# Kernel tuning notes

Hardware: AMD Instinct MI355X
Metric: run time of the kernel (lower is better)

## Reference

```python
import jax, jax.numpy as jnp
import numpy as np

N_NODES = 50000
N_EDGES = 1000000


def _edge_conv(x, src, dst, W, b, n_nodes):
    """PyG EdgeConv: msg = nn(cat([x_i, x_j - x_i])), aggr=max over incoming edges."""
    xi = x[dst]                      # [E, C] target features
    xj = x[src]                      # [E, C] source features
    m = jnp.concatenate([xi, xj - xi], axis=-1)          # [E, 2C]
    m = jax.nn.relu(m @ W + b)                           # [E, C_out]
    out = jax.ops.segment_max(m, dst, num_segments=n_nodes)  # [N, C_out]
    # empty segments produce -inf; PyG fills with 0
    return jnp.where(jnp.isfinite(out), out, 0.0)


def setup_inputs() -> dict:
    key = jax.random.key(0)
    ks = jax.random.split(key, 12)
    x = jax.random.normal(ks[0], (N_NODES, 3), dtype=jnp.float32)
    edge_index = jax.random.randint(ks[1], (2, N_EDGES), 0, N_NODES, dtype=jnp.int64)

    def lin(k, fan_in, fan_out):
        s = 1.0 / np.sqrt(fan_in)
        kw, kb = jax.random.split(k)
        W = jax.random.uniform(kw, (fan_in, fan_out), jnp.float32, -s, s)
        b = jax.random.uniform(kb, (fan_out,), jnp.float32, -s, s)
        return W, b

    W1, b1 = lin(ks[2], 6, 64)       # conv1 MLP([3*2, 64])
    W2, b2 = lin(ks[3], 128, 128)    # conv2 MLP([64*2, 128])
    W3, b3 = lin(ks[4], 256, 512)    # conv3 MLP([128*2, 512])
    W4, b4 = lin(ks[5], 512, 256)    # lin1 MLP([512, 256])
    W5, b5 = lin(ks[6], 256, 3)      # lin1 final Linear(256, 3)
    return {"x": x, "edge_index": edge_index,
            "W1": W1, "b1": b1, "W2": W2, "b2": b2, "W3": W3, "b3": b3,
            "W4": W4, "b4": b4, "W5": W5, "b5": b5}


def reference(x, edge_index, W1, b1, W2, b2, W3, b3, W4, b4, W5, b5):
    src = edge_index[0]  # x_j
    dst = edge_index[1]  # x_i (aggregation target)
    n = x.shape[0]
    x1 = _edge_conv(x, src, dst, W1, b1, n)    # [N, 64]
    x2 = _edge_conv(x1, src, dst, W2, b2, n)   # [N, 128]
    x3 = _edge_conv(x2, src, dst, W3, b3, n)   # [N, 512]
    x4 = jax.nn.relu(x3 @ W4 + b4) @ W5 + b5   # [N, 3]
    return x + x4
```

## Files before the change

kernel.cpp:

```cpp
#include <hip/hip_runtime.h>

static constexpr int NN = 50000;
static constexpr int NE = 1000000;

typedef short bf16x8 __attribute__((ext_vector_type(8)));
typedef float f32x4 __attribute__((ext_vector_type(4)));
typedef unsigned short u16x2 __attribute__((ext_vector_type(2)));

__device__ inline float bf2f_raw(unsigned short u) {
    return __uint_as_float(((unsigned int)u) << 16);
}
__device__ inline unsigned short f2bf(float f) {
    unsigned int u = __float_as_uint(f);
    u += 0x7fffu + ((u >> 16) & 1u);
    return (unsigned short)(u >> 16);
}
__device__ inline unsigned short f2bfs(float f) {
    unsigned short b = f2bf(f);
    return (b & 0x8000u) ? (unsigned short)(~b) : (unsigned short)(b | 0x8000u);
}
__device__ inline float unsrt2f(unsigned short v) {
    unsigned short b = (v & 0x8000u) ? (unsigned short)(v ^ 0x8000u)
                                     : (unsigned short)(~v);
    return bf2f_raw(b);
}
__device__ inline unsigned int pkmax(unsigned int a, unsigned int b) {
    u16x2 r = __builtin_elementwise_max(__builtin_bit_cast(u16x2, a),
                                        __builtin_bit_cast(u16x2, b));
    return __builtin_bit_cast(unsigned int, r);
}
__device__ inline uint4 pkmax4(uint4 a, uint4 b) {
    a.x = pkmax(a.x, b.x); a.y = pkmax(a.y, b.y);
    a.z = pkmax(a.z, b.z); a.w = pkmax(a.w, b.w);
    return a;
}
__device__ inline unsigned int pack2(float f0, float f1) {
    return (unsigned int)f2bf(f0) | ((unsigned int)f2bf(f1) << 16);
}
__device__ inline unsigned int addrelu2t(unsigned int a, unsigned int t) {
    float t0 = unsrt2f((unsigned short)(t & 0xffffu));
    float t1 = unsrt2f((unsigned short)(t >> 16));
    float f0 = fmaxf(bf2f_raw((unsigned short)(a & 0xffffu)) + t0, 0.f);
    float f1 = fmaxf(bf2f_raw((unsigned short)(a >> 16)) + t1, 0.f);
    return pack2(f0, f1);
}


__global__ void setup_kernel(const float* __restrict__ x, const float* __restrict__ W1,
                             const float* __restrict__ b1, const float* __restrict__ b5,
                             const float* __restrict__ W2, const float* __restrict__ W3,
                             const float* __restrict__ W4,
                             unsigned short* __restrict__ as1, float* __restrict__ out,
                             int* __restrict__ deg, int* __restrict__ cursor,
                             unsigned short* __restrict__ Bt2,
                             unsigned short* __restrict__ Bt3,
                             unsigned short* __restrict__ W4t) {
    int t = blockIdx.x * blockDim.x + threadIdx.x;
    if (t < NN * 128) {
        int i = t >> 7, c = t & 127;
        float x0 = x[i * 3 + 0], x1 = x[i * 3 + 1], x2 = x[i * 3 + 2];
        if (c < 64) {
            float v = x0 * (W1[c] - W1[192 + c]) + x1 * (W1[64 + c] - W1[256 + c]) +
                      x2 * (W1[128 + c] - W1[320 + c]) + b1[c];
            as1[t] = f2bf(v);
        } else {
            int cs = c - 64;
            float v = x0 * W1[192 + cs] + x1 * W1[256 + cs] + x2 * W1[320 + cs];
            as1[t] = f2bfs(v);
        }
        return;
    }
    t -= NN * 128;
    if (t < NN * 3) { out[t] = x[t] + b5[t % 3]; return; }
    t -= NN * 3;
    if (t < NN) { deg[t] = 0; return; }
    t -= NN;
    if (t < NN) { cursor[t] = 0; return; }
    t -= NN;
    if (t < 8192) {
        int k = t / 128, c = t % 128;
        float wt = W2[k * 128 + c];
        float wb = W2[(64 + k) * 128 + c];
        Bt2[c * 64 + k] = f2bf(wt - wb);
        Bt2[(128 + c) * 64 + k] = f2bf(wb);
        return;
    }
    t -= 8192;
    if (t < 65536) {
        int k = t / 512, c = t % 512;
        float wt = W3[k * 512 + c];
        float wb = W3[(128 + k) * 512 + c];
        Bt3[c * 128 + k] = f2bf(wt - wb);
        Bt3[(512 + c) * 128 + k] = f2bf(wb);
        return;
    }
    t -= 65536;
    if (t < 131072) {
        int k = t / 256, n = t % 256;
        W4t[n * 512 + k] = f2bf(W4[k * 256 + n]);
    }
}


__global__ void hist_kernel(const int* __restrict__ dst, int* __restrict__ deg) {
    int e = blockIdx.x * blockDim.x + threadIdx.x;
    if (e < NE) atomicAdd(&deg[dst[e]], 1);
}

__global__ __launch_bounds__(1024) void scan_kernel(const int* __restrict__ deg,
                                                    int* __restrict__ rowstart) {
    __shared__ int wave_sums[16];
    constexpr int CH = (NN + 1023) / 1024;
    int tid = threadIdx.x;
    int lane = tid & 63;
    int wave = tid >> 6;
    int base = tid * CH;
    int vals[CH];
    int sum = 0;
    #pragma unroll
    for (int i = 0; i < CH; ++i) {
        int idx = base + i;
        vals[i] = (idx < NN) ? deg[idx] : 0;
        sum += vals[i];
    }
    int x = sum;
    #pragma unroll
    for (int off = 1; off < 64; off <<= 1) {
        int y = __shfl_up(x, off);
        if (lane >= off) x += y;
    }
    if (lane == 63) wave_sums[wave] = x;
    __syncthreads();
    if (wave == 0 && lane < 16) {
        int s = wave_sums[lane];
        #pragma unroll
        for (int off = 1; off < 16; off <<= 1) {
            int y = __shfl_up(s, off);
            if (lane >= off) s += y;
        }
        wave_sums[lane] = s;
    }
    __syncthreads();
    int run = (wave ? wave_sums[wave - 1] : 0) + x - sum;
    #pragma unroll
    for (int i = 0; i < CH; ++i) {
        int idx = base + i;
        if (idx < NN) rowstart[idx] = run;
        run += vals[i];
    }
    if (tid == 1023) rowstart[NN] = run;
}

__global__ void scatter_kernel(const int* __restrict__ src, const int* __restrict__ dst,
                               const int* __restrict__ rowstart, int* __restrict__ cursor,
                               int* __restrict__ csr) {
    int e = blockIdx.x * blockDim.x + threadIdx.x;
    if (e < NE) {
        int d = dst[e];
        int pos = atomicAdd(&cursor[d], 1);
        csr[rowstart[d] + pos] = src[e];
    }
}


__global__ __launch_bounds__(256) void edge_fused_conv1_kernel(
    const unsigned short* __restrict__ as, const int* __restrict__ rowstart,
    const int* __restrict__ csr, unsigned short* __restrict__ x1) {
    int wid = (blockIdx.x * 256 + threadIdx.x) >> 6;
    int lane = threadIdx.x & 63;
    if (wid >= NN) return;
    int e0 = __builtin_amdgcn_readfirstlane(rowstart[wid]);
    int e1 = __builtin_amdgcn_readfirstlane(rowstart[wid + 1]);
    int nedge = e1 - e0;
    unsigned int mA = 0u, mB = 0u;
    if (nedge > 0) {
        int last = nedge - 1;
        for (int e = 0; e < nedge; e += 16) {
            int jj[16];
            #pragma unroll
            for (int k = 0; k < 16; ++k) {
                int idx = e + k; if (idx > last) idx = last;
                jj[k] = __builtin_amdgcn_readfirstlane(csr[e0 + idx]);
            }
            unsigned int v[16];
            #pragma unroll
            for (int k = 0; k < 16; ++k)
                v[k] = *(const unsigned short*)(as + (size_t)jj[k] * 128 + 64 + lane);
            #pragma unroll
            for (int k = 0; k < 16; ++k) {
                if (k & 1) mB = mB > v[k] ? mB : v[k];
                else       mA = mA > v[k] ? mA : v[k];
            }
        }
    }
    unsigned int m = mA > mB ? mA : mB;
    unsigned short a = as[(size_t)wid * 128 + lane];
    float t = unsrt2f((unsigned short)m);
    float f = fmaxf(bf2f_raw(a) + t, 0.f);
    x1[(size_t)wid * 64 + lane] = f2bf(f);
}


__global__ __launch_bounds__(256) void ef128_a2_kernel(
    const unsigned short* __restrict__ s2, const unsigned short* __restrict__ x1,
    const int* __restrict__ rowstart, const int* __restrict__ csr,
    const unsigned short* __restrict__ Bt2a, const float* __restrict__ b2,
    unsigned short* __restrict__ x2) {
    __shared__ __align__(16) unsigned short A2[16][136];
    int tid = threadIdx.x;
    int wave = tid >> 6, lane = tid & 63;
    int quad = lane >> 4, l16 = lane & 15;
    int tilebase = blockIdx.x * 16;

    bf16x8 afr[2];
    #pragma unroll
    for (int kc = 0; kc < 2; ++kc)
        afr[kc] = *(const bf16x8*)&x1[(size_t)(tilebase + l16) * 64 + kc * 32 + quad * 8];

    {
        int colbase = wave * 32;
        f32x4 acc[2] = {};
        #pragma unroll
        for (int kc = 0; kc < 2; ++kc) {
            #pragma unroll
            for (int nt = 0; nt < 2; ++nt) {
                int col = colbase + nt * 16 + l16;
                bf16x8 bfr = *(const bf16x8*)&Bt2a[(size_t)col * 64 + kc * 32 + quad * 8];
                acc[nt] = __builtin_amdgcn_mfma_f32_16x16x32_bf16(afr[kc], bfr, acc[nt], 0, 0, 0);
            }
        }
        #pragma unroll
        for (int nt = 0; nt < 2; ++nt) {
            int col = colbase + nt * 16 + l16;
            float bv = b2[col];
            #pragma unroll
            for (int r = 0; r < 4; ++r)
                A2[quad * 4 + r][col] = f2bf(acc[nt][r] + bv);
        }
    }

    unsigned int m[4];
    for (int i = 0; i < 4; ++i) {
        int node = tilebase + wave * 4 + i;
        int e0 = __builtin_amdgcn_readfirstlane(rowstart[node]);
        int e1 = __builtin_amdgcn_readfirstlane(rowstart[node + 1]);
        int nedge = e1 - e0;
        unsigned int mA = 0u, mB = 0u;
        if (nedge > 0) {
            int last = nedge - 1;
            for (int e = 0; e < nedge; e += 16) {
                int jj[16];
                #pragma unroll
                for (int k = 0; k < 16; ++k) {
                    int idx = e + k; if (idx > last) idx = last;
                    jj[k] = __builtin_amdgcn_readfirstlane(csr[e0 + idx]);
                }
                unsigned int v[16];
                #pragma unroll
                for (int k = 0; k < 16; ++k)
                    v[k] = *(const unsigned int*)(s2 + (size_t)jj[k] * 128 + lane * 2);
                #pragma unroll
                for (int k = 0; k < 16; ++k) {
                    if (k & 1) mB = pkmax(mB, v[k]);
                    else       mA = pkmax(mA, v[k]);
                }
            }
        }
        m[i] = pkmax(mA, mB);
    }
    __syncthreads();

    #pragma unroll
    for (int i = 0; i < 4; ++i) {
        int row = wave * 4 + i;
        unsigned int av = *(const unsigned int*)&A2[row][lane * 2];
        *(unsigned int*)(x2 + (size_t)(tilebase + row) * 128 + lane * 2) =
            addrelu2t(av, m[i]);
    }
}


__global__ __launch_bounds__(256) void ef512_w5_kernel(
    const unsigned short* __restrict__ s3, const unsigned short* __restrict__ x2,
    const int* __restrict__ rowstart, const int* __restrict__ csr,
    const unsigned short* __restrict__ Bt3a, const float* __restrict__ b3,
    const unsigned short* __restrict__ W4t,
    const float* __restrict__ b4, const float* __restrict__ W5,
    float* __restrict__ out) {
    __shared__ __align__(16) unsigned short X[16][520];
    int tid = threadIdx.x;
    int wave = tid >> 6, lane = tid & 63;
    int quad = lane >> 4, l16 = lane & 15;
    int tilebase = blockIdx.x * 16;

    bf16x8 afr[4];
    #pragma unroll
    for (int kc = 0; kc < 4; ++kc)
        afr[kc] = *(const bf16x8*)&x2[(size_t)(tilebase + l16) * 128 + kc * 32 + quad * 8];

    {
        int colbase = wave * 128;
        f32x4 acc3[8] = {};
        #pragma unroll
        for (int kc = 0; kc < 4; ++kc) {
            #pragma unroll
            for (int nt = 0; nt < 8; ++nt) {
                int col = colbase + nt * 16 + l16;
                bf16x8 bfr = *(const bf16x8*)&Bt3a[(size_t)col * 128 + kc * 32 + quad * 8];
                acc3[nt] = __builtin_amdgcn_mfma_f32_16x16x32_bf16(afr[kc], bfr, acc3[nt], 0, 0, 0);
            }
        }
        #pragma unroll
        for (int nt = 0; nt < 8; ++nt) {
            int col = colbase + nt * 16 + l16;
            float bv = b3[col];
            #pragma unroll
            for (int r = 0; r < 4; ++r)
                X[quad * 4 + r][col] = f2bf(acc3[nt][r] + bv);
        }
    }

    uint4 m[4];
    for (int i = 0; i < 4; ++i) {
        int node = tilebase + wave * 4 + i;
        int e0 = __builtin_amdgcn_readfirstlane(rowstart[node]);
        int e1 = __builtin_amdgcn_readfirstlane(rowstart[node + 1]);
        int nedge = e1 - e0;
        uint4 mA = make_uint4(0u, 0u, 0u, 0u), mB = make_uint4(0u, 0u, 0u, 0u);
        if (nedge > 0) {
            int last = nedge - 1;
            for (int e = 0; e < nedge; e += 8) {
                int jj[8];
                #pragma unroll
                for (int k = 0; k < 8; ++k) {
                    int idx = e + k; if (idx > last) idx = last;
                    jj[k] = __builtin_amdgcn_readfirstlane(csr[e0 + idx]);
                }
                uint4 v[8];
                #pragma unroll
                for (int k = 0; k < 8; ++k)
                    v[k] = *(const uint4*)(s3 + (size_t)jj[k] * 512 + lane * 8);
                #pragma unroll
                for (int k = 0; k < 8; ++k) {
                    if (k & 1) mB = pkmax4(mB, v[k]);
                    else       mA = pkmax4(mA, v[k]);
                }
            }
        }
        m[i] = pkmax4(mA, mB);
    }
    __syncthreads();

    #pragma unroll
    for (int i = 0; i < 4; ++i) {
        int row = wave * 4 + i;
        uint4 av = *(const uint4*)&X[row][lane * 8];
        uint4 o;
        o.x = addrelu2t(av.x, m[i].x);
        o.y = addrelu2t(av.y, m[i].y);
        o.z = addrelu2t(av.z, m[i].z);
        o.w = addrelu2t(av.w, m[i].w);
        *(uint4*)&X[row][lane * 8] = o;
    }
    __syncthreads();

    int colbase = wave * 64;
    f32x4 acc4[4] = {};
    for (int kc = 0; kc < 16; ++kc) {
        bf16x8 a4 = *(const bf16x8*)&X[l16][kc * 32 + quad * 8];
        #pragma unroll
        for (int nt = 0; nt < 4; ++nt) {
            int col = colbase + nt * 16 + l16;
            bf16x8 bfr = *(const bf16x8*)&W4t[(size_t)col * 512 + kc * 32 + quad * 8];
            acc4[nt] = __builtin_amdgcn_mfma_f32_16x16x32_bf16(a4, bfr, acc4[nt], 0, 0, 0);
        }
    }
    float b4v[4], w5r[4][3];
    #pragma unroll
    for (int nt = 0; nt < 4; ++nt) {
        int col = colbase + nt * 16 + l16;
        b4v[nt] = b4[col];
        w5r[nt][0] = W5[col * 3 + 0];
        w5r[nt][1] = W5[col * 3 + 1];
        w5r[nt][2] = W5[col * 3 + 2];
    }
    #pragma unroll
    for (int r = 0; r < 4; ++r) {
        int row = tilebase + quad * 4 + r;
        float p0 = 0.f, p1 = 0.f, p2 = 0.f;
        #pragma unroll
        for (int nt = 0; nt < 4; ++nt) {
            float h = fmaxf(acc4[nt][r] + b4v[nt], 0.f);
            p0 += h * w5r[nt][0];
            p1 += h * w5r[nt][1];
            p2 += h * w5r[nt][2];
        }
        #pragma unroll
        for (int mm = 8; mm; mm >>= 1) {
            p0 += __shfl_xor(p0, mm);
            p1 += __shfl_xor(p1, mm);
            p2 += __shfl_xor(p2, mm);
        }
        if (l16 == 0) {
            atomicAdd(&out[row * 3 + 0], p0);
            atomicAdd(&out[row * 3 + 1], p1);
            atomicAdd(&out[row * 3 + 2], p2);
        }
    }
}


template<int K, int NT>
__global__ __launch_bounds__(256) void mfma_gemm_nloop_kernel(
    const unsigned short* __restrict__ A, const unsigned short* __restrict__ Bt,
    const float* __restrict__ bias, int bias_n,
    unsigned short* __restrict__ C, int M) {
    constexpr int KC = K / 32;
    constexpr int N = NT * 128;
    __shared__ __align__(16) unsigned short Asl[KC][128 * 40];
    __shared__ __align__(16) unsigned short Bsl[128 * 40];
    int tid = threadIdx.x;
    int mbase = blockIdx.x * 128;
    int wave = tid >> 6, lane = tid & 63;
    int wm = (wave >> 1) * 64, wn = (wave & 1) * 64;
    int quad = lane >> 4, l16 = lane & 15;

    #pragma unroll
    for (int c = tid; c < KC * 512; c += 256) {
        int kc = c >> 9, rem = c & 511;
        int r = rem >> 2, kk = (rem & 3) * 8;
        uint4 va = make_uint4(0u, 0u, 0u, 0u);
        int gr = mbase + r;
        if (gr < M) va = *(const uint4*)&A[(size_t)gr * K + kc * 32 + kk];
        *(uint4*)&Asl[kc][r * 40 + kk] = va;
    }

    for (int nt = 0; nt < NT; ++nt) {
        int nbase = nt * 128;
        f32x4 acc[4][4] = {};
        for (int kc = 0; kc < KC; ++kc) {
            __syncthreads();
            #pragma unroll
            for (int h = 0; h < 2; ++h) {
                int c = tid + h * 256;
                int r = c >> 2, kk = (c & 3) * 8;
                uint4 vb = *(const uint4*)&Bt[(size_t)(nbase + r) * K + kc * 32 + kk];
                *(uint4*)&Bsl[r * 40 + kk] = vb;
            }
            __syncthreads();
            bf16x8 af[4], bfr[4];
            #pragma unroll
            for (int tt = 0; tt < 4; ++tt) {
                af[tt]  = *(const bf16x8*)&Asl[kc][(wm + tt * 16 + l16) * 40 + quad * 8];
                bfr[tt] = *(const bf16x8*)&Bsl[(wn + tt * 16 + l16) * 40 + quad * 8];
            }
            #pragma unroll
            for (int mt = 0; mt < 4; ++mt)
                #pragma unroll
                for (int ntt = 0; ntt < 4; ++ntt)
                    acc[mt][ntt] = __builtin_amdgcn_mfma_f32_16x16x32_bf16(
                        af[mt], bfr[ntt], acc[mt][ntt], 0, 0, 0);
        }
        #pragma unroll
        for (int mt = 0; mt < 4; ++mt) {
            #pragma unroll
            for (int r = 0; r < 4; ++r) {
                int row = mbase + wm + mt * 16 + quad * 4 + r;
                if (row >= M) continue;
                #pragma unroll
                for (int ntt = 0; ntt < 4; ++ntt) {
                    int col = nbase + wn + ntt * 16 + l16;
                    float v = acc[mt][ntt][r];
                    unsigned short o;
                    if (col < bias_n) o = f2bf(v + bias[col]);
                    else o = f2bfs(v);
                    C[(size_t)row * N + col] = o;
                }
            }
        }
    }
}

__global__ void fallback_copy_kernel(const float* __restrict__ x, float* __restrict__ out) {
    int t = blockIdx.x * blockDim.x + threadIdx.x;
    if (t < NN * 3) out[t] = x[t];
}


extern "C" void kernel_launch(void* const* d_in, const int* in_sizes, int n_in,
                              void* d_out, int out_size, void* d_ws, size_t ws_size,
                              hipStream_t stream) {
    const float* x  = (const float*)d_in[0];
    const int*   ei = (const int*)d_in[1];
    const float* W1 = (const float*)d_in[2];
    const float* b1 = (const float*)d_in[3];
    const float* W2 = (const float*)d_in[4];
    const float* b2 = (const float*)d_in[5];
    const float* W3 = (const float*)d_in[6];
    const float* b3 = (const float*)d_in[7];
    const float* W4 = (const float*)d_in[8];
    const float* b4 = (const float*)d_in[9];
    const float* W5 = (const float*)d_in[10];
    const float* b5 = (const float*)d_in[11];
    float* out = (float*)d_out;

    char* p = (char*)d_ws;
    auto alloc = [&](size_t bytes) -> void* {
        void* r = (void*)p;
        p += (bytes + 255) & ~(size_t)255;
        return r;
    };
    int* deg      = (int*)alloc((size_t)NN * 4);
    int* rowstart = (int*)alloc((size_t)(NN + 1) * 4);
    int* cursor   = (int*)alloc((size_t)NN * 4);
    int* csr      = (int*)alloc((size_t)NE * 4);
    unsigned short* Bt2 = (unsigned short*)alloc(256 * 64 * 2);
    unsigned short* Bt3 = (unsigned short*)alloc(1024 * 128 * 2);
    unsigned short* W4t = (unsigned short*)alloc(256 * 512 * 2);
    unsigned short* x1 = (unsigned short*)alloc((size_t)NN * 64 * 2);
    unsigned short* x2 = (unsigned short*)alloc((size_t)NN * 128 * 2);
    unsigned short* as_slab = (unsigned short*)alloc((size_t)NN * 512 * 2);
    size_t need = (size_t)(p - (char*)d_ws);
    if (ws_size < need) {
        fallback_copy_kernel<<<(NN * 3 + 255) / 256, 256, 0, stream>>>(x, out);
        return;
    }

    const int* src = ei;
    const int* dst = ei + NE;

    constexpr int SETUP_T = NN * 128 + NN * 3 + NN + NN + 8192 + 65536 + 131072;
    setup_kernel<<<(SETUP_T + 255) / 256, 256, 0, stream>>>(
        x, W1, b1, b5, W2, W3, W4, as_slab, out, deg, cursor, Bt2, Bt3, W4t);

    hist_kernel<<<(NE + 255) / 256, 256, 0, stream>>>(dst, deg);
    scan_kernel<<<1, 1024, 0, stream>>>(deg, rowstart);
    scatter_kernel<<<(NE + 255) / 256, 256, 0, stream>>>(src, dst, rowstart, cursor, csr);

    edge_fused_conv1_kernel<<<12500, 256, 0, stream>>>(as_slab, rowstart, csr, x1);

    mfma_gemm_nloop_kernel<64, 1><<<391, 256, 0, stream>>>(
        x1, Bt2 + 128 * 64, b2, 0, as_slab, NN);
    ef128_a2_kernel<<<NN / 16, 256, 0, stream>>>(
        as_slab, x1, rowstart, csr, Bt2, b2, x2);

    mfma_gemm_nloop_kernel<128, 4><<<391, 256, 0, stream>>>(
        x2, Bt3 + 512 * 128, b3, 0, as_slab, NN);

    ef512_w5_kernel<<<NN / 16, 256, 0, stream>>>(
        as_slab, x2, rowstart, csr, Bt3, b3, W4t, b4, W5, out);
}
```

Before: 565.9 us.

## Compute conv3 self term in the GEMM kernel instead of the edge-fused kernel

The conv3 A-part (x_i·(W_top−W_bot)+b) is now computed by the node GEMM, which widens its output to 1024 columns per node stored in a doubled slab. The ef512 kernel no longer runs its own 16x512 MFMA on x2. It reads the precomputed self term from global memory alongside the gathered B-part and drops one barrier. In exchange the slab doubles to 100 MB, the gather reads use a 2 KB row stride, and the GEMM writes twice as much data.

```diff
diff --git a/kernel.cpp b/kernel.cpp
--- a/kernel.cpp
+++ b/kernel.cpp
@@ -281,46 +281,15 @@
 
 
 __global__ __launch_bounds__(256) void ef512_w5_kernel(
-    const unsigned short* __restrict__ s3, const unsigned short* __restrict__ x2,
-    const int* __restrict__ rowstart, const int* __restrict__ csr,
-    const unsigned short* __restrict__ Bt3a, const float* __restrict__ b3,
-    const unsigned short* __restrict__ W4t,
+    const unsigned short* __restrict__ as, const int* __restrict__ rowstart,
+    const int* __restrict__ csr, const unsigned short* __restrict__ W4t,
     const float* __restrict__ b4, const float* __restrict__ W5,
     float* __restrict__ out) {
     __shared__ __align__(16) unsigned short X[16][520];
-    int tid = threadIdx.x;
-    int wave = tid >> 6, lane = tid & 63;
+    int wave = threadIdx.x >> 6, lane = threadIdx.x & 63;
     int quad = lane >> 4, l16 = lane & 15;
     int tilebase = blockIdx.x * 16;
 
-    bf16x8 afr[4];
-    #pragma unroll
-    for (int kc = 0; kc < 4; ++kc)
-        afr[kc] = *(const bf16x8*)&x2[(size_t)(tilebase + l16) * 128 + kc * 32 + quad * 8];
-
-    {
-        int colbase = wave * 128;
-        f32x4 acc3[8] = {};
-        #pragma unroll
-        for (int kc = 0; kc < 4; ++kc) {
-            #pragma unroll
-            for (int nt = 0; nt < 8; ++nt) {
-                int col = colbase + nt * 16 + l16;
-                bf16x8 bfr = *(const bf16x8*)&Bt3a[(size_t)col * 128 + kc * 32 + quad * 8];
-                acc3[nt] = __builtin_amdgcn_mfma_f32_16x16x32_bf16(afr[kc], bfr, acc3[nt], 0, 0, 0);
-            }
-        }
-        #pragma unroll
-        for (int nt = 0; nt < 8; ++nt) {
-            int col = colbase + nt * 16 + l16;
-            float bv = b3[col];
-            #pragma unroll
-            for (int r = 0; r < 4; ++r)
-                X[quad * 4 + r][col] = f2bf(acc3[nt][r] + bv);
-        }
-    }
-
-    uint4 m[4];
     for (int i = 0; i < 4; ++i) {
         int node = tilebase + wave * 4 + i;
         int e0 = __builtin_amdgcn_readfirstlane(rowstart[node]);
@@ -339,7 +308,7 @@
                 uint4 v[8];
                 #pragma unroll
                 for (int k = 0; k < 8; ++k)
-                    v[k] = *(const uint4*)(s3 + (size_t)jj[k] * 512 + lane * 8);
+                    v[k] = *(const uint4*)(as + (size_t)jj[k] * 1024 + 512 + lane * 8);
                 #pragma unroll
                 for (int k = 0; k < 8; ++k) {
                     if (k & 1) mB = pkmax4(mB, v[k]);
@@ -347,20 +316,14 @@
                 }
             }
         }
-        m[i] = pkmax4(mA, mB);
-    }
-    __syncthreads();
-
-    #pragma unroll
-    for (int i = 0; i < 4; ++i) {
-        int row = wave * 4 + i;
-        uint4 av = *(const uint4*)&X[row][lane * 8];
+        uint4 m = pkmax4(mA, mB);
+        uint4 av = *(const uint4*)(as + (size_t)node * 1024 + lane * 8);
         uint4 o;
-        o.x = addrelu2t(av.x, m[i].x);
-        o.y = addrelu2t(av.y, m[i].y);
-        o.z = addrelu2t(av.z, m[i].z);
-        o.w = addrelu2t(av.w, m[i].w);
-        *(uint4*)&X[row][lane * 8] = o;
+        o.x = addrelu2t(av.x, m.x);
+        o.y = addrelu2t(av.y, m.y);
+        o.z = addrelu2t(av.z, m.z);
+        o.w = addrelu2t(av.w, m.w);
+        *(uint4*)&X[wave * 4 + i][lane * 8] = o;
     }
     __syncthreads();
 
@@ -519,7 +482,7 @@
     unsigned short* W4t = (unsigned short*)alloc(256 * 512 * 2);
     unsigned short* x1 = (unsigned short*)alloc((size_t)NN * 64 * 2);
     unsigned short* x2 = (unsigned short*)alloc((size_t)NN * 128 * 2);
-    unsigned short* as_slab = (unsigned short*)alloc((size_t)NN * 512 * 2);
+    unsigned short* as_slab = (unsigned short*)alloc((size_t)NN * 1024 * 2);
     size_t need = (size_t)(p - (char*)d_ws);
     if (ws_size < need) {
         fallback_copy_kernel<<<(NN * 3 + 255) / 256, 256, 0, stream>>>(x, out);
@@ -544,9 +507,9 @@
     ef128_a2_kernel<<<NN / 16, 256, 0, stream>>>(
         as_slab, x1, rowstart, csr, Bt2, b2, x2);
 
-    mfma_gemm_nloop_kernel<128, 4><<<391, 256, 0, stream>>>(
-        x2, Bt3 + 512 * 128, b3, 0, as_slab, NN);
+    mfma_gemm_nloop_kernel<128, 8><<<391, 256, 0, stream>>>(
+        x2, Bt3, b3, 512, as_slab, NN);
 
     ef512_w5_kernel<<<NN / 16, 256, 0, stream>>>(
-        as_slab, x2, rowstart, csr, Bt3, b3, W4t, b4, W5, out);
-}
+        as_slab, rowstart, csr, W4t, b4, W5, out);
+}
```

After: 608.4 us. +7.5%, slower.
